# Kernel optimization log

Hardware: AMD Instinct MI355X
Metric: run time of the kernel (lower is better)

## Reference

```python
import jax, jax.numpy as jnp
import numpy as np

BETA = 50.0
SIGMA = 5.0


def l2_normalize(x, axis=1):
    # matches torch: norm = (sum(x^2) + 1e-6) ** 0.5
    return x / jnp.sqrt(jnp.sum(x * x, axis=axis, keepdims=True) + 1e-6)


def matching_layer(f1, f2):
    # corr[b, j, i] = <f2[:, j], f1[:, i]>, shaped (b, h2*w2, h1, w1)
    f1 = l2_normalize(f1, 1)
    f2 = l2_normalize(f2, 1)
    b, c, h, w = f1.shape
    corr = jnp.einsum('bcj,bci->bji', f2.reshape(b, c, h * w), f1.reshape(b, c, h * w))
    return jax.nn.relu(corr).reshape(b, h * w, h, w)


def kernel_soft_argmax(corr, beta=BETA, sigma=SIGMA):
    b, hw, h, w = corr.shape
    # gaussian kernel centered at argmax over the target-position axis (dim 1)
    idx = jnp.argmax(corr, axis=1)                      # (b, h, w)
    idx_y = (idx // w).astype(corr.dtype)[:, None, None]  # (b,1,1,h,w)
    idx_x = (idx % w).astype(corr.dtype)[:, None, None]
    xs = jnp.arange(w, dtype=corr.dtype).reshape(1, 1, w, 1, 1)
    ys = jnp.arange(h, dtype=corr.dtype).reshape(1, h, 1, 1, 1)
    gauss = jnp.exp(-((xs - idx_x) ** 2 + (ys - idx_y) ** 2) / (2.0 * sigma ** 2))
    corr = gauss.reshape(b, hw, h, w) * corr
    # softmax with temperature over dim 1 (stable: subtract max, then exp(beta*x))
    m = jnp.max(corr, axis=1, keepdims=True)
    e = jnp.exp(beta * (corr - m))
    p = e / jnp.sum(e, axis=1, keepdims=True)
    p = p.reshape(b, h, w, h, w)
    x_normal = jnp.linspace(-1.0, 1.0, w, dtype=corr.dtype).reshape(1, w, 1, 1)
    y_normal = jnp.linspace(-1.0, 1.0, h, dtype=corr.dtype).reshape(1, h, 1, 1)
    grid_x = jnp.sum(jnp.sum(p, axis=1) * x_normal, axis=1, keepdims=True)  # (b,1,h,w)
    grid_y = jnp.sum(jnp.sum(p, axis=2) * y_normal, axis=1, keepdims=True)  # (b,1,h,w)
    return grid_x, grid_y


def find_correspondence(corr):
    grid_x, grid_y = kernel_soft_argmax(corr)
    grid = jnp.concatenate([jnp.transpose(grid_x, (0, 2, 3, 1)),
                            jnp.transpose(grid_y, (0, 2, 3, 1))], axis=3)  # (b,h,w,2)
    # faithful to source: flow = grid_x - grid_x == zeros
    flow = jnp.concatenate([grid_x - grid_x, grid_y - grid_y], axis=1)  # (b,2,h,w)
    return grid, flow


def setup_inputs() -> dict:
    key = jax.random.key(0)
    k1, k2, k3, k4 = jax.random.split(key, 4)
    return {
        'src_feat3': jax.random.normal(k1, (2, 1024, 64, 64), dtype=jnp.float32),
        'tgt_feat3': jax.random.normal(k2, (2, 1024, 64, 64), dtype=jnp.float32),
        'src_feat4': jax.random.normal(k3, (2, 2048, 64, 64), dtype=jnp.float32),
        'tgt_feat4': jax.random.normal(k4, (2, 2048, 64, 64), dtype=jnp.float32),
    }


def reference(src_feat3, tgt_feat3, src_feat4, tgt_feat4):
    corr3 = matching_layer(src_feat3, tgt_feat3)  # (b, hw, h, w)
    corr4 = matching_layer(src_feat4, tgt_feat4)
    b, hw, h, w = corr3.shape
    corr_s2t = l2_normalize(corr3 * corr4, axis=1)
    # transpose source/target axes for t2s
    corr3_t = jnp.transpose(corr3.reshape(b, hw, hw), (0, 2, 1)).reshape(b, hw, h, w)
    corr4_t = jnp.transpose(corr4.reshape(b, hw, hw), (0, 2, 1)).reshape(b, hw, h, w)
    corr_t2s = l2_normalize(corr3_t * corr4_t, axis=1)
    grid_s2t, flow_s2t = find_correspondence(corr_s2t)
    grid_t2s, flow_t2s = find_correspondence(corr_t2s)
    return grid_s2t, flow_s2t, grid_t2s, flow_t2s
```

## Files before the change

kernel.cpp:

```cpp
#include <hip/hip_runtime.h>
#include <math.h>

#define HW 4096
#define FIXUP_THR 4e-3f

typedef _Float16 half8_t __attribute__((ext_vector_type(8)));
typedef _Float16 half4_t __attribute__((ext_vector_type(4)));
typedef float f32x4 __attribute__((ext_vector_type(4)));

__global__ __launch_bounds__(256) void transpose_b(
    const float* __restrict__ s3f, const float* __restrict__ t3f,
    const float* __restrict__ s4f, const float* __restrict__ t4f,
    _Float16* __restrict__ P, float* __restrict__ part, int b) {
    __shared__ float tile[64][65];
    const int t = threadIdx.x;
    int blk = blockIdx.x;
    const float* f;
    _Float16* out;
    float* pt;
    int C;
    if (blk < 2048) {
        C = 1024;
        if (blk < 1024) { f = t3f; out = P;            pt = part;          }
        else            { f = s3f; out = P + 4194304;  pt = part + 65536;  blk -= 1024; }
    } else {
        C = 2048;
        if (blk < 4096) { f = t4f; out = P + 8388608;  pt = part + 131072; blk -= 2048; }
        else            { f = s4f; out = P + 16777216; pt = part + 262144; blk -= 4096; }
    }
    const int p0 = (blk & 63) * 64;
    const int c0 = (blk >> 6) * 64;
    const int cblk = blk >> 6;
    const float* src = f + ((size_t)b * C + c0) * HW + p0;
    {
        const int cl = t >> 4;
        const int pl = (t & 15) * 4;
#pragma unroll
        for (int it = 0; it < 4; ++it) {
            float4 v = *(const float4*)(src + (size_t)(cl + it * 16) * HW + pl);
            tile[cl + it * 16][pl + 0] = v.x;
            tile[cl + it * 16][pl + 1] = v.y;
            tile[cl + it * 16][pl + 2] = v.z;
            tile[cl + it * 16][pl + 3] = v.w;
        }
    }
    __syncthreads();
    const int pr = t >> 3;
    const int cb = (t & 7) * 8;
#pragma unroll
    for (int it = 0; it < 2; ++it) {
        const int p = pr + it * 32;
        union { _Float16 h[8]; float4 v4; } H;
        float ssq = 0.f;
#pragma unroll
        for (int u = 0; u < 8; ++u) {
            float v = tile[cb + u][p];
            H.h[u] = (_Float16)v;
            ssq = fmaf(v, v, ssq);
        }
        *(float4*)(out + (size_t)(p0 + p) * C + c0 + cb) = H.v4;
        ssq += __shfl_down(ssq, 4);
        ssq += __shfl_down(ssq, 2);
        ssq += __shfl_down(ssq, 1);
        if ((t & 7) == 0) pt[(size_t)cblk * 4096 + p0 + p] = ssq;
    }
}

__global__ __launch_bounds__(256) void norm_finalize_b(const float* __restrict__ part,
                                                       float* __restrict__ inv, int b) {
    const int idx = blockIdx.x * 256 + threadIdx.x;
    const int tensor = idx >> 12;
    const int pos = idx & 4095;
    const int nblk[4] = {16, 16, 32, 32};
    const int poff[4] = {0, 65536, 131072, 262144};
    const int ivoff[4] = {8192, 0, 24576, 16384};
    const float* pt = part + poff[tensor] + pos;
    float s = 0.f;
    const int n = nblk[tensor];
    for (int k = 0; k < n; ++k) s += pt[(size_t)k * 4096];
    inv[ivoff[tensor] + b * 4096 + pos] = 1.0f / sqrtf(s + 1e-6f);
}

__global__ __launch_bounds__(256, 2) void corr_fused(
    const _Float16* __restrict__ A3, const _Float16* __restrict__ B3,
    const _Float16* __restrict__ A4, const _Float16* __restrict__ B4,
    const float* __restrict__ invA3, const float* __restrict__ invB3,
    const float* __restrict__ invA4, const float* __restrict__ invB4,
    _Float16* __restrict__ M, _Float16* __restrict__ MT, int b) {
    __shared__ char lds[65536];
    const int tid = threadIdx.x;
    const int i0 = blockIdx.x * 128;
    const int j0 = blockIdx.y * 128;
    const int lane = tid & 63;
    const int w = tid >> 6;
    const int wj = (w >> 1) * 64, wi = (w & 1) * 64;
    const int quad = lane >> 4;

    int offA[2][4], offB[2][4];
#pragma unroll
    for (int f = 0; f < 4; ++f) {
        int jr = wj + f * 16 + (lane & 15);
        int baseA = jr * 128 + ((quad ^ (jr & 3)) << 4);
        int xkA = ((jr >> 2) & 1) << 6;
        offA[0][f] = baseA + xkA;
        offA[1][f] = baseA + (64 ^ xkA);
        int ir = wi + f * 16 + (lane & 15);
        int baseB = 16384 + ir * 128 + ((quad ^ (ir & 3)) << 4);
        int xkB = ((ir >> 2) & 1) << 6;
        offB[0][f] = baseB + xkB;
        offB[1][f] = baseB + (64 ^ xkB);
    }

    int srow[8], selem[8];
#pragma unroll
    for (int s = 0; s < 8; ++s) {
        int g = s * 256 + tid;
        srow[s] = (g >> 3) & 127;
        selem[s] = ((g & 7) ^ (srow[s] & 7)) << 3;
    }

    const _Float16* s3p[8];
    const _Float16* s4p[8];
#pragma unroll
    for (int s = 0; s < 8; ++s) {
        if (s < 4) {
            s3p[s] = A3 + (size_t)(j0 + srow[s]) * 1024 + selem[s];
            s4p[s] = A4 + (size_t)(j0 + srow[s]) * 2048 + selem[s];
        } else {
            s3p[s] = B3 + (size_t)(i0 + srow[s]) * 1024 + selem[s];
            s4p[s] = B4 + (size_t)(i0 + srow[s]) * 2048 + selem[s];
        }
    }

    half4_t v3p[4][4];
    f32x4 acc[4][4] = {};

    auto stage = [&](int buf, const _Float16** sp) {
#pragma unroll
        for (int s = 0; s < 8; ++s) {
            __builtin_amdgcn_global_load_lds(
                (const __attribute__((address_space(1))) void*)(sp[s]),
                (__attribute__((address_space(3))) void*)(lds + (buf << 15) +
                                                          (s * 256 + tid) * 16),
                16, 0, 0);
            sp[s] += 64;
        }
    };
    auto compute = [&](int buf) {
        const int bo = buf << 15;
#pragma unroll
        for (int st = 0; st < 2; ++st) {
            half8_t a[4], bb[4];
#pragma unroll
            for (int f = 0; f < 4; ++f) {
                a[f] = *(const half8_t*)(lds + bo + offA[st][f]);
                bb[f] = *(const half8_t*)(lds + bo + offB[st][f]);
            }
#pragma unroll
            for (int fy = 0; fy < 4; ++fy)
#pragma unroll
                for (int fx = 0; fx < 4; ++fx)
                    acc[fy][fx] = __builtin_amdgcn_mfma_f32_16x16x32_f16(
                        a[fy], bb[fx], acc[fy][fx], 0, 0, 0);
        }
    };

    stage(0, s3p);
    __syncthreads();
    int cur = 0;
#pragma unroll 1
    for (int kt = 0; kt < 16; ++kt) {
        if (kt < 15) stage(cur ^ 1, s3p);
        else         stage(cur ^ 1, s4p);
        compute(cur);
        __syncthreads();
        cur ^= 1;
    }

    {
        const int ib = i0 + wi + (lane & 15);
        float sB[4];
#pragma unroll
        for (int fx = 0; fx < 4; ++fx) sB[fx] = invB3[b * 4096 + ib + fx * 16];
#pragma unroll
        for (int fy = 0; fy < 4; ++fy) {
            const int jb = j0 + wj + fy * 16 + quad * 4;
            float sA[4];
#pragma unroll
            for (int r = 0; r < 4; ++r) sA[r] = invA3[b * 4096 + jb + r];
#pragma unroll
            for (int fx = 0; fx < 4; ++fx)
#pragma unroll
                for (int r = 0; r < 4; ++r) {
                    v3p[fy][fx][r] =
                        (_Float16)fmaxf(acc[fy][fx][r] * sA[r] * sB[fx], 0.f);
                    acc[fy][fx][r] = 0.f;
                }
        }
    }

#pragma unroll 1
    for (int kt = 0; kt < 32; ++kt) {
        if (kt < 31) stage(cur ^ 1, s4p);
        compute(cur);
        __syncthreads();
        cur ^= 1;
    }

    const int ib = i0 + wi + (lane & 15);
    float sB[4];
#pragma unroll
    for (int fx = 0; fx < 4; ++fx) sB[fx] = invB4[b * 4096 + ib + fx * 16];
#pragma unroll
    for (int fy = 0; fy < 4; ++fy) {
        const int jb = j0 + wj + fy * 16 + quad * 4;
        float sA[4];
#pragma unroll
        for (int r = 0; r < 4; ++r) sA[r] = invA4[b * 4096 + jb + r];
#pragma unroll
        for (int fx = 0; fx < 4; ++fx) {
            const int ii = ib + fx * 16;
            union { _Float16 h[4]; double d; } pk;
#pragma unroll
            for (int r = 0; r < 4; ++r) {
                float v = fmaxf(acc[fy][fx][r] * sA[r] * sB[fx], 0.f) *
                          (float)v3p[fy][fx][r];
                M[((size_t)b * HW + (jb + r)) * HW + ii] = (_Float16)v;
                pk.h[r] = (_Float16)v;
            }
            *(double*)(MT + ((size_t)b * HW + ii) * HW + jb) = pk.d;
        }
    }
}

__device__ __forceinline__ void top2_merge(float& a1, int& ai1, float& a2, int& ai2,
                                           float b1, int bi1, float b2, int bi2) {
    float n1, n2;
    int ni1, ni2;
    bool bfirst = (b1 > a1) || (b1 == a1 && bi1 < ai1);
    if (bfirst) {
        n1 = b1; ni1 = bi1;
        if (a1 > b2 || (a1 == b2 && ai1 < bi2)) { n2 = a1; ni2 = ai1; }
        else { n2 = b2; ni2 = bi2; }
    } else {
        n1 = a1; ni1 = ai1;
        if (b1 > a2 || (b1 == a2 && bi1 < ai2)) { n2 = b1; ni2 = bi1; }
        else { n2 = a2; ni2 = ai2; }
    }
    a1 = n1; ai1 = ni1; a2 = n2; ai2 = ni2;
}

__global__ __launch_bounds__(256, 6) void soft_argmax(
    const _Float16* __restrict__ M, const _Float16* __restrict__ MT,
    float* __restrict__ out,
    const float* __restrict__ s3, const float* __restrict__ t3,
    const float* __restrict__ s4, const float* __restrict__ t4,
    const float* __restrict__ inv) {
    __shared__ _Float16 bufh[HW];
    __shared__ float lf[3072];
    __shared__ float gtab[128];
    __shared__ float wsA[4], wsB[4], wsC[4];
    __shared__ int wiA[4], wiB[4];
    __shared__ int cnd[64];
    __shared__ int ncnd;
    __shared__ float bestE;
    __shared__ int bestI;
    const int tid = threadIdx.x;
    const int lane = tid & 63;
    const int wv = tid >> 6;
    const int b = blockIdx.y;
    const int line = blockIdx.x;
    const int colmode = blockIdx.z;

    const float* cf3 = colmode ? t3 : s3;
    const float* lf3 = colmode ? s3 : t3;
    const float* cf4 = colmode ? t4 : s4;
    const float* lf4 = colmode ? s4 : t4;
    const float* invc3 = inv + (colmode ? 8192 : 0);
    const float* invl3 = inv + (colmode ? 0 : 8192);
    const float* invc4 = inv + (colmode ? 24576 : 16384);
    const float* invl4 = inv + (colmode ? 16384 : 24576);

    const _Float16* src = (colmode ? MT : M) + ((size_t)b * HW + line) * HW;
    const half8_t* s8 = (const half8_t*)src;

    float ss = 0.f, v1 = -1.f, v2 = -1.f;
    int i1 = 0, i2 = 0;
#pragma unroll
    for (int it = 0; it < 2; ++it) {
        const int j8 = tid + it * 256;
        half8_t h = s8[j8];
        *(half8_t*)(bufh + j8 * 8) = h;
#pragma unroll
        for (int u = 0; u < 8; ++u) {
            float v = (float)h[u];
            int j = j8 * 8 + u;
            ss = fmaf(v, v, ss);
            if (v > v1) { v2 = v1; i2 = i1; v1 = v; i1 = j; }
            else if (v > v2) { v2 = v; i2 = j; }
        }
    }
#pragma unroll
    for (int m = 1; m < 64; m <<= 1) {
        ss += __shfl_xor(ss, m);
        float b1 = __shfl_xor(v1, m); int bi1 = __shfl_xor(i1, m);
        float b2 = __shfl_xor(v2, m); int bi2 = __shfl_xor(i2, m);
        top2_merge(v1, i1, v2, i2, b1, bi1, b2, bi2);
    }
    if (lane == 0) { wsA[wv] = ss; wsB[wv] = v1; wiA[wv] = i1; wsC[wv] = v2; wiB[wv] = i2; }
    __syncthreads();
    float ssq = wsA[0] + wsA[1] + wsA[2] + wsA[3];
    float m1 = wsB[0], m2 = wsC[0];
    int mi1 = wiA[0], mi2 = wiB[0];
#pragma unroll
    for (int k = 1; k < 4; ++k)
        top2_merge(m1, mi1, m2, mi2, wsB[k], wiA[k], wsC[k], wiB[k]);
    const float inv_l = 1.0f / sqrtf(ssq + 1e-6f);
    const float vmax = m1 * inv_l;
    int amax = mi1;
    (void)mi2;

    const float cut = m1 - FIXUP_THR * m1;
    if (m2 >= cut) {
        if (tid == 0) { ncnd = 0; bestE = -1.f; bestI = 1 << 30; }
        __syncthreads();
        for (int j = tid; j < HW; j += 256)
            if ((float)bufh[j] >= cut) {
                int k = atomicAdd(&ncnd, 1);
                if (k < 64) cnd[k] = j;
            }
        for (int c = tid; c < 1024; c += 256)
            lf[c] = lf3[((size_t)b * 1024 + c) * HW + line];
        for (int c = tid; c < 2048; c += 256)
            lf[1024 + c] = lf4[((size_t)b * 2048 + c) * HW + line];
        __syncthreads();
        int nc = ncnd < 64 ? ncnd : 64;
#pragma unroll 1
        for (int k = 0; k < nc; ++k) {
            int jc = cnd[k];
            float d3 = 0.f, d4 = 0.f;
            for (int c = tid; c < 1024; c += 256)
                d3 = fmaf(cf3[((size_t)b * 1024 + c) * HW + jc], lf[c], d3);
            for (int c = tid; c < 2048; c += 256)
                d4 = fmaf(cf4[((size_t)b * 2048 + c) * HW + jc], lf[1024 + c], d4);
#pragma unroll
            for (int m = 1; m < 64; m <<= 1) {
                d3 += __shfl_xor(d3, m);
                d4 += __shfl_xor(d4, m);
            }
            if (lane == 0) { wsA[wv] = d3; wsB[wv] = d4; }
            __syncthreads();
            if (tid == 0) {
                float s3d = wsA[0] + wsA[1] + wsA[2] + wsA[3];
                float s4d = wsB[0] + wsB[1] + wsB[2] + wsB[3];
                float e3 = fmaxf(s3d * invc3[b * 4096 + jc] * invl3[b * 4096 + line], 0.f);
                float e4 = fmaxf(s4d * invc4[b * 4096 + jc] * invl4[b * 4096 + line], 0.f);
                float e = e3 * e4;
                if (e > bestE || (e == bestE && jc < bestI)) { bestE = e; bestI = jc; }
            }
            __syncthreads();
        }
        amax = bestI;
    }

    const float ax = (float)(amax & 63);
    const float ay = (float)(amax >> 6);

    if (tid < 128) {
        float d = (float)(tid & 63) - ((tid < 64) ? ax : ay);
        gtab[tid] = __expf(-d * d * 0.02f);
    }
    __syncthreads();

    float se = 0.f, sx = 0.f, sy = 0.f;
#pragma unroll
    for (int it = 0; it < 2; ++it) {
        const int j8 = tid + it * 256;
        half8_t h = *(const half8_t*)(bufh + j8 * 8);
        const int x0 = (j8 & 7) * 8;
        const int y2 = j8 >> 3;
        const float gyi = gtab[64 + y2] * inv_l;
        const float yn = fmaf((float)y2, 2.0f / 63.0f, -1.0f);
        float sec = 0.f;
#pragma unroll
        for (int u = 0; u < 8; ++u) {
            float v = gtab[x0 + u] * (float)h[u] * gyi;
            float e = __expf(50.0f * (v - vmax));
            sec += e;
            sx = fmaf(e, fmaf((float)(x0 + u), 2.0f / 63.0f, -1.0f), sx);
        }
        se += sec;
        sy = fmaf(sec, yn, sy);
    }
#pragma unroll
    for (int m = 1; m < 64; m <<= 1) {
        se += __shfl_xor(se, m);
        sx += __shfl_xor(sx, m);
        sy += __shfl_xor(sy, m);
    }
    if (lane == 0) { wsA[wv] = se; wsB[wv] = sx; wsC[wv] = sy; }
    __syncthreads();
    if (tid == 0) {
        float S = wsA[0] + wsA[1] + wsA[2] + wsA[3];
        float X = wsB[0] + wsB[1] + wsB[2] + wsB[3];
        float Y = wsC[0] + wsC[1] + wsC[2] + wsC[3];
        float gx = X / S;
        float gy = Y / S;
        size_t gbase = colmode ? 0 : 32768;
        size_t fbase = colmode ? 16384 : 49152;
        size_t p = gbase + ((size_t)b * HW + line) * 2;
        out[p] = gx;
        out[p + 1] = gy;
        out[fbase + (size_t)(b * 2 + 0) * HW + line] = 0.f;
        out[fbase + (size_t)(b * 2 + 1) * HW + line] = 0.f;
    }
}

extern "C" void kernel_launch(void* const* d_in, const int* in_sizes, int n_in,
                              void* d_out, int out_size, void* d_ws, size_t ws_size,
                              hipStream_t stream) {
    const float* s3 = (const float*)d_in[0];
    const float* t3 = (const float*)d_in[1];
    const float* s4 = (const float*)d_in[2];
    const float* t4 = (const float*)d_in[3];
    float* out = (float*)d_out;
    char* base = (char*)d_ws;

    float* inv = (float*)base;
    float* part = (float*)(base + 131072);
    _Float16* M16 = (_Float16*)(base + 1703936);
    _Float16* MT16 = (_Float16*)(base + 68812800);
    _Float16* P = (_Float16*)(base + 135921664);

    dim3 gg(32, 32);
    for (int b = 0; b < 2; ++b) {
        transpose_b<<<6144, 256, 0, stream>>>(s3, t3, s4, t4, P, part, b);
        norm_finalize_b<<<64, 256, 0, stream>>>(part, inv, b);
        corr_fused<<<gg, 256, 0, stream>>>(P, P + 4194304, P + 8388608, P + 16777216,
                                           inv + 8192, inv + 0, inv + 24576, inv + 16384,
                                           M16, MT16, b);
    }

    dim3 rg(4096, 2, 2);
    soft_argmax<<<rg, 256, 0, stream>>>(M16, MT16, out, s3, t3, s4, t4, inv);
}
```

Baseline: 572.3 us.

## Stage transposed correlation tile in LDS and hold soft-argmax rows in registers

The correlation kernel now writes each transposed output fragment into shared memory first. After a barrier, it stores full coalesced 16-byte rows of MT instead of scattered 8-byte writes. The soft-argmax kernel moves to 512 threads so each thread holds one half8 chunk of the row in registers, which removes the shared-memory row buffer and the reload in the second pass. The cost is an extra barrier and reuse of the GEMM's LDS in the correlation kernel, plus wider block reductions over 8 waves.

Result: slower. 628.7 us (+9.8%).

```diff
diff --git a/kernel.cpp b/kernel.cpp
--- a/kernel.cpp
+++ b/kernel.cpp
@@ -207,19 +207,23 @@
         cur ^= 1;
     }
 
+    _Float16* ldsT = (_Float16*)lds;
     const int ib = i0 + wi + (lane & 15);
+    const int liB = wi + (lane & 15);
     float sB[4];
 #pragma unroll
     for (int fx = 0; fx < 4; ++fx) sB[fx] = invB4[b * 4096 + ib + fx * 16];
 #pragma unroll
     for (int fy = 0; fy < 4; ++fy) {
         const int jb = j0 + wj + fy * 16 + quad * 4;
+        const int ljb = wj + fy * 16 + quad * 4;
         float sA[4];
 #pragma unroll
         for (int r = 0; r < 4; ++r) sA[r] = invA4[b * 4096 + jb + r];
 #pragma unroll
         for (int fx = 0; fx < 4; ++fx) {
             const int ii = ib + fx * 16;
+            const int li = liB + fx * 16;
             union { _Float16 h[4]; double d; } pk;
 #pragma unroll
             for (int r = 0; r < 4; ++r) {
@@ -228,7 +232,18 @@
                 M[((size_t)b * HW + (jb + r)) * HW + ii] = (_Float16)v;
                 pk.h[r] = (_Float16)v;
             }
-            *(double*)(MT + ((size_t)b * HW + ii) * HW + jb) = pk.d;
+            *(double*)(ldsT + li * 136 + ljb) = pk.d;
+        }
+    }
+    __syncthreads();
+    {
+        const int rr = tid >> 4;
+        const int cc = (tid & 15) * 8;
+#pragma unroll
+        for (int q = 0; q < 8; ++q) {
+            const int r = rr + q * 16;
+            *(float4*)(MT + ((size_t)b * HW + i0 + r) * HW + j0 + cc) =
+                *(const float4*)(ldsT + r * 136 + cc);
         }
     }
 }
@@ -250,17 +265,16 @@
     a1 = n1; ai1 = ni1; a2 = n2; ai2 = ni2;
 }
 
-__global__ __launch_bounds__(256, 6) void soft_argmax(
+__global__ __launch_bounds__(512, 8) void soft_argmax(
     const _Float16* __restrict__ M, const _Float16* __restrict__ MT,
     float* __restrict__ out,
     const float* __restrict__ s3, const float* __restrict__ t3,
     const float* __restrict__ s4, const float* __restrict__ t4,
     const float* __restrict__ inv) {
-    __shared__ _Float16 bufh[HW];
     __shared__ float lf[3072];
     __shared__ float gtab[128];
-    __shared__ float wsA[4], wsB[4], wsC[4];
-    __shared__ int wiA[4], wiB[4];
+    __shared__ float wsA[8], wsB[8], wsC[8];
+    __shared__ int wiA[8], wiB[8];
     __shared__ int cnd[64];
     __shared__ int ncnd;
     __shared__ float bestE;
@@ -282,23 +296,17 @@
     const float* invl4 = inv + (colmode ? 16384 : 24576);
 
     const _Float16* src = (colmode ? MT : M) + ((size_t)b * HW + line) * HW;
-    const half8_t* s8 = (const half8_t*)src;
+    const half8_t h = ((const half8_t*)src)[tid];
 
     float ss = 0.f, v1 = -1.f, v2 = -1.f;
     int i1 = 0, i2 = 0;
 #pragma unroll
-    for (int it = 0; it < 2; ++it) {
-        const int j8 = tid + it * 256;
-        half8_t h = s8[j8];
-        *(half8_t*)(bufh + j8 * 8) = h;
-#pragma unroll
-        for (int u = 0; u < 8; ++u) {
-            float v = (float)h[u];
-            int j = j8 * 8 + u;
-            ss = fmaf(v, v, ss);
-            if (v > v1) { v2 = v1; i2 = i1; v1 = v; i1 = j; }
-            else if (v > v2) { v2 = v; i2 = j; }
-        }
+    for (int u = 0; u < 8; ++u) {
+        float v = (float)h[u];
+        int j = tid * 8 + u;
+        ss = fmaf(v, v, ss);
+        if (v > v1) { v2 = v1; i2 = i1; v1 = v; i1 = j; }
+        else if (v > v2) { v2 = v; i2 = j; }
     }
 #pragma unroll
     for (int m = 1; m < 64; m <<= 1) {
@@ -309,11 +317,13 @@
     }
     if (lane == 0) { wsA[wv] = ss; wsB[wv] = v1; wiA[wv] = i1; wsC[wv] = v2; wiB[wv] = i2; }
     __syncthreads();
-    float ssq = wsA[0] + wsA[1] + wsA[2] + wsA[3];
+    float ssq = 0.f;
+#pragma unroll
+    for (int k = 0; k < 8; ++k) ssq += wsA[k];
     float m1 = wsB[0], m2 = wsC[0];
     int mi1 = wiA[0], mi2 = wiB[0];
 #pragma unroll
-    for (int k = 1; k < 4; ++k)
+    for (int k = 1; k < 8; ++k)
         top2_merge(m1, mi1, m2, mi2, wsB[k], wiA[k], wsC[k], wiB[k]);
     const float inv_l = 1.0f / sqrtf(ssq + 1e-6f);
     const float vmax = m1 * inv_l;
@@ -324,14 +334,15 @@
     if (m2 >= cut) {
         if (tid == 0) { ncnd = 0; bestE = -1.f; bestI = 1 << 30; }
         __syncthreads();
-        for (int j = tid; j < HW; j += 256)
-            if ((float)bufh[j] >= cut) {
+#pragma unroll
+        for (int u = 0; u < 8; ++u)
+            if ((float)h[u] >= cut) {
                 int k = atomicAdd(&ncnd, 1);
-                if (k < 64) cnd[k] = j;
+                if (k < 64) cnd[k] = tid * 8 + u;
             }
-        for (int c = tid; c < 1024; c += 256)
+        for (int c = tid; c < 1024; c += 512)
             lf[c] = lf3[((size_t)b * 1024 + c) * HW + line];
-        for (int c = tid; c < 2048; c += 256)
+        for (int c = tid; c < 2048; c += 512)
             lf[1024 + c] = lf4[((size_t)b * 2048 + c) * HW + line];
         __syncthreads();
         int nc = ncnd < 64 ? ncnd : 64;
@@ -339,9 +350,9 @@
         for (int k = 0; k < nc; ++k) {
             int jc = cnd[k];
             float d3 = 0.f, d4 = 0.f;
-            for (int c = tid; c < 1024; c += 256)
+            for (int c = tid; c < 1024; c += 512)
                 d3 = fmaf(cf3[((size_t)b * 1024 + c) * HW + jc], lf[c], d3);
-            for (int c = tid; c < 2048; c += 256)
+            for (int c = tid; c < 2048; c += 512)
                 d4 = fmaf(cf4[((size_t)b * 2048 + c) * HW + jc], lf[1024 + c], d4);
 #pragma unroll
             for (int m = 1; m < 64; m <<= 1) {
@@ -351,8 +362,9 @@
             if (lane == 0) { wsA[wv] = d3; wsB[wv] = d4; }
             __syncthreads();
             if (tid == 0) {
-                float s3d = wsA[0] + wsA[1] + wsA[2] + wsA[3];
-                float s4d = wsB[0] + wsB[1] + wsB[2] + wsB[3];
+                float s3d = 0.f, s4d = 0.f;
+#pragma unroll
+                for (int q = 0; q < 8; ++q) { s3d += wsA[q]; s4d += wsB[q]; }
                 float e3 = fmaxf(s3d * invc3[b * 4096 + jc] * invl3[b * 4096 + line], 0.f);
                 float e4 = fmaxf(s4d * invc4[b * 4096 + jc] * invl4[b * 4096 + line], 0.f);
                 float e = e3 * e4;
@@ -372,26 +384,19 @@
     }
     __syncthreads();
 
-    float se = 0.f, sx = 0.f, sy = 0.f;
-#pragma unroll
-    for (int it = 0; it < 2; ++it) {
-        const int j8 = tid + it * 256;
-        half8_t h = *(const half8_t*)(bufh + j8 * 8);
-        const int x0 = (j8 & 7) * 8;
-        const int y2 = j8 >> 3;
-        const float gyi = gtab[64 + y2] * inv_l;
-        const float yn = fmaf((float)y2, 2.0f / 63.0f, -1.0f);
-        float sec = 0.f;
-#pragma unroll
-        for (int u = 0; u < 8; ++u) {
-            float v = gtab[x0 + u] * (float)h[u] * gyi;
-            float e = __expf(50.0f * (v - vmax));
-            sec += e;
-            sx = fmaf(e, fmaf((float)(x0 + u), 2.0f / 63.0f, -1.0f), sx);
-        }
-        se += sec;
-        sy = fmaf(sec, yn, sy);
-    }
+    const int x0 = (tid & 7) * 8;
+    const int y2 = tid >> 3;
+    const float gyi = gtab[64 + y2] * inv_l;
+    const float yn = fmaf((float)y2, 2.0f / 63.0f, -1.0f);
+    float se = 0.f, sx = 0.f;
+#pragma unroll
+    for (int u = 0; u < 8; ++u) {
+        float v = gtab[x0 + u] * (float)h[u] * gyi;
+        float e = __expf(50.0f * (v - vmax));
+        se += e;
+        sx = fmaf(e, fmaf((float)(x0 + u), 2.0f / 63.0f, -1.0f), sx);
+    }
+    float sy = se * yn;
 #pragma unroll
     for (int m = 1; m < 64; m <<= 1) {
         se += __shfl_xor(se, m);
@@ -401,9 +406,9 @@
     if (lane == 0) { wsA[wv] = se; wsB[wv] = sx; wsC[wv] = sy; }
     __syncthreads();
     if (tid == 0) {
-        float S = wsA[0] + wsA[1] + wsA[2] + wsA[3];
-        float X = wsB[0] + wsB[1] + wsB[2] + wsB[3];
-        float Y = wsC[0] + wsC[1] + wsC[2] + wsC[3];
+        float S = 0.f, X = 0.f, Y = 0.f;
+#pragma unroll
+        for (int k = 0; k < 8; ++k) { S += wsA[k]; X += wsB[k]; Y += wsC[k]; }
         float gx = X / S;
         float gy = Y / S;
         size_t gbase = colmode ? 0 : 32768;
@@ -442,5 +447,5 @@
     }
 
     dim3 rg(4096, 2, 2);
-    soft_argmax<<<rg, 256, 0, stream>>>(M16, MT16, out, s3, t3, s4, t4, inv);
-}
+    soft_argmax<<<rg, 512, 0, stream>>>(M16, MT16, out, s3, t3, s4, t4, inv);
+}
```
